# Performance work log

Measured on AMD Instinct MI355X. Metric: run time of the kernel, lower is better.

The kernel has to match this reference:

```python
import jax, jax.numpy as jnp
import numpy as np

N = 100000      # nodes
E = 1600000     # edges (avg degree 16)
IN = 64         # in_feats
OUT = 64        # out_feats per head
H = 4           # heads
SLOPE = 0.2     # leaky relu negative slope


def setup_inputs() -> dict:
    key = jax.random.key(0)
    ks = jax.random.split(key, 6)
    feat = jax.random.normal(ks[0], (N, IN), dtype=jnp.float32)
    # xavier-ish scale for weights
    W_weight = jax.random.normal(ks[1], (OUT * H, IN), dtype=jnp.float32) * (2.0 / (IN + OUT * H)) ** 0.5
    W_bias = jnp.zeros((OUT * H,), dtype=jnp.float32)
    a_l = jax.random.normal(ks[2], (1, OUT, H), dtype=jnp.float32) * 0.1
    a_r = jax.random.normal(ks[3], (1, OUT, H), dtype=jnp.float32) * 0.1
    row = jax.random.randint(ks[4], (E,), 0, N, dtype=jnp.int32)
    col = jax.random.randint(ks[5], (E,), 0, N, dtype=jnp.int32)
    return {"feat": feat, "W_weight": W_weight, "W_bias": W_bias,
            "a_l": a_l, "a_r": a_r, "row": row, "col": col}


def reference(feat, W_weight, W_bias, a_l, a_r, row, col):
    n = feat.shape[0]
    # linear projection -> [N, OUT, H]
    Z = (feat @ W_weight.T + W_bias).reshape(n, OUT, H)
    # per-node attention logits [N, H]
    e_l = (Z * a_l).sum(axis=1)
    e_r = (Z * a_r).sum(axis=1)
    # edge scores + leaky relu [E, H]
    e = e_l[row] + e_r[col]
    a = jnp.where(e > 0, e, SLOPE * e)
    # segment softmax over incoming edges of each destination row
    m = jax.ops.segment_max(a, row, num_segments=n)          # [N, H]
    ex = jnp.exp(a - m[row])                                  # [E, H]
    s = jax.ops.segment_sum(ex, row, num_segments=n)          # [N, H]
    alpha = ex / s[row]                                       # [E, H]
    # weighted aggregation: out[i,:,h] = sum_{e: row[e]=i} alpha[e,h] * Z[col[e],:,h]
    msg = alpha[:, None, :] * Z[col]                          # [E, OUT, H]
    out = jax.ops.segment_sum(msg, row, num_segments=n)       # [N, OUT, H]
    return out.reshape(n, -1)
```

## Files before the change

### kernel.cpp

```cpp
#include <hip/hip_runtime.h>
#include <stdint.h>

#define SLOPE  0.2f
#define PN     64
#define CAP    48
#define SCAP   16
#define SBMAX  512
#define ESMAX  3200
#define BINS   1600

typedef float    f32x4 __attribute__((ext_vector_type(4)));
typedef _Float16 h16x2 __attribute__((ext_vector_type(2)));

union FU { float f; unsigned int u; };
union HU { unsigned int u; h16x2 h; };
__device__ __forceinline__ float ubits(unsigned int u) { FU c; c.u = u; return c.f; }

__global__ __launch_bounds__(256) void front_kernel(
    const int* __restrict__ row, const int* __restrict__ col,
    int* __restrict__ cnt_sub,
    unsigned int* __restrict__ subreg,
    const float4* __restrict__ feat4, const float* __restrict__ W,
    const float* __restrict__ bias, const float* __restrict__ a_l,
    const float* __restrict__ a_r,
    uint2* __restrict__ featb2, float* __restrict__ el, float* __restrict__ er,
    unsigned int* __restrict__ WtHu, float* __restrict__ biasP,
    int E, int ES, int NBK, int N, int SC, int PJ)
{
    __shared__ char smemRaw[33024];

    int b = blockIdx.x;
    int t = threadIdx.x;

    if (b < SC) {
        unsigned int* stage = (unsigned int*)smemRaw;
        int* hist = (int*)(smemRaw + 12800);
        int* ofs  = (int*)(smemRaw + 19200);
        int* cur  = (int*)(smemRaw + 25600);
        int* part = (int*)(smemRaw + 32000);

        int blk = b;
        int e0 = blk * ES;
        int e1 = min(e0 + ES, E);
        int tot = e1 - e0;

        for (int p = t; p < BINS; p += 256) hist[p] = 0;
        __syncthreads();

        for (int e = e0 + t; e < e1; e += 256) {
            int r = __builtin_nontemporal_load(&row[e]);
            atomicAdd(&hist[r >> 6], 1);
        }
        __syncthreads();

        int lc[7]; int loc = 0;
        #pragma unroll
        for (int q = 0; q < 7; q++) {
            int bb = t * 7 + q;
            int v = (bb < BINS) ? hist[bb] : 0;
            lc[q] = loc; loc += v;
        }
        part[t] = loc;
        __syncthreads();
        for (int off = 1; off < 256; off <<= 1) {
            int v = (t >= off) ? part[t - off] : 0;
            __syncthreads();
            part[t] += v;
            __syncthreads();
        }
        int pbase = (t > 0) ? part[t - 1] : 0;
        #pragma unroll
        for (int q = 0; q < 7; q++) {
            int bb = t * 7 + q;
            if (bb < BINS) { ofs[bb] = pbase + lc[q]; cur[bb] = pbase + lc[q]; }
        }
        __syncthreads();

        for (int e = e0 + t; e < e1; e += 256) {
            int r = __builtin_nontemporal_load(&row[e]);
            int c = __builtin_nontemporal_load(&col[e]);
            int pos = atomicAdd(&cur[r >> 6], 1);
            stage[pos] = (unsigned)c | ((unsigned)(r & 63) << 20);
        }
        __syncthreads();

        unsigned int* dst = subreg + (size_t)blk * NBK * SCAP;
        int mx = max(tot - 1, 0);
        for (int p = t; p < NBK * SCAP; p += 256) {
            int bk = p >> 4, j = p & 15;
            int idx = ofs[bk] + j;
            dst[p] = stage[min(idx, mx)];
        }
        for (int p = t; p < NBK; p += 256)
            cnt_sub[(size_t)blk * NBK + p] = min(hist[p], SCAP);
        return;
    }
    if (b < SC + PJ) {
        float (*fT)[68]  = (float(*)[68])smemRaw;
        float (*WlS)[68] = (float(*)[68])(smemRaw + 17408);
        float* blS       = (float*)(smemRaw + 17408 + 2176);

        int nodeBase = (b - SC) * PN;

        for (int p = t; p < PN * 16; p += 256) {
            int n = p >> 4, kq = p & 15;
            int gn = nodeBase + n;
            float4 v = make_float4(0.f, 0.f, 0.f, 0.f);
            if (gn < N) v = feat4[(size_t)gn * 16 + kq];
            fT[kq * 4 + 0][n] = v.x; fT[kq * 4 + 1][n] = v.y;
            fT[kq * 4 + 2][n] = v.z; fT[kq * 4 + 3][n] = v.w;
            if (gn < N) {
                HU u0, u1;
                u0.h = (h16x2){ (_Float16)v.x, (_Float16)v.y };
                u1.h = (h16x2){ (_Float16)v.z, (_Float16)v.w };
                featb2[(size_t)gn * 16 + kq] = make_uint2(u0.u, u1.u);
            }
        }
        for (int r = 0; r < 2; r++) {
            int id = t + 256 * r;
            int x = id >> 6, k = id & 63, h = x & 3;
            const float* v = (x < 4) ? a_l : a_r;
            float s = 0.f;
            for (int d = 0; d < 64; d++) {
                int o = d * 4 + h;
                s += v[o] * W[o * 64 + k];
            }
            WlS[x][k] = s;
        }
        if (t < 8) {
            int h = t & 3;
            const float* v = (t < 4) ? a_l : a_r;
            float s = 0.f;
            for (int d = 0; d < 64; d++) { int o = d * 4 + h; s += v[o] * bias[o]; }
            blS[t] = s;
        }
        __syncthreads();

        for (int r = 0; r < 2; r++) {
            int id = t + 256 * r;
            int n = id >> 3, x = id & 7;
            int gn = nodeBase + n;
            if (gn < N) {
                float e = blS[x];
                #pragma unroll 8
                for (int k = 0; k < 64; k++) e += fT[k][n] * WlS[x][k];
                if (x < 4) el[(size_t)gn * 4 + x] = e;
                else       er[(size_t)gn * 4 + (x - 4)] = e;
            }
        }
        return;
    }
    if (b < SC + PJ + 32) {
        int g = (b - SC - PJ) * 256 + t;
        int kk = g >> 8, cp = g & 255;
        int o = (cp & 63) * 4 + (cp >> 6);
        HU u;
        u.h = (h16x2){ (_Float16)W[o * 64 + 2 * kk], (_Float16)W[o * 64 + 2 * kk + 1] };
        WtHu[kk * 256 + cp] = u.u;
        return;
    }
    {
        int cp = t;
        int o = (cp & 63) * 4 + (cp >> 6);
        biasP[cp] = bias[o];
    }
}

__global__ __launch_bounds__(1024) void gat_aggregate(
    const uint2* __restrict__ featb2,
    const float* __restrict__ el, const float* __restrict__ er,
    const int* __restrict__ cnt_sub, const unsigned int* __restrict__ subreg,
    uint2* __restrict__ agg, int* __restrict__ deg,
    int N, int NBK, int SB)
{
    __shared__ int      cntL[64];
    __shared__ unsigned listL[64 * CAP];
    __shared__ float    aL[16][64];
    __shared__ int      segC[SBMAX];

    int t = threadIdx.x, lane = t & 63, w = t >> 6;
    int bk = blockIdx.x;
    int nodeBase = bk << 6;

    for (int p = t; p < 64 * CAP / 4; p += 1024)
        *(uint4*)&listL[p * 4] = make_uint4(0u, 0u, 0u, 0u);
    if (t < 64) cntL[t] = 0;
    for (int p = t; p < SB; p += 1024) segC[p] = cnt_sub[(size_t)p * NBK + bk];
    __syncthreads();

    for (int p = t; p < SB * SCAP; p += 1024) {
        int blk = p >> 4, j = p & 15;
        if (j < segC[blk]) {
            unsigned wd = subreg[((size_t)blk * NBK + bk) * SCAP + j];
            int nl = wd >> 20;
            int pos = atomicAdd(&cntL[nl], 1);
            if (pos < CAP) listL[nl * CAP + pos] = wd & 0xFFFFFu;
        }
    }
    __syncthreads();

    int eL = lane >> 2, hh = lane & 3;
    int hsel = lane >> 4, kq = lane & 15;

    for (int u = 0; u < 4; u++) {
        int nl = w * 4 + u;
        int i = nodeBase + nl;
        if (i >= N) break;
        int dg = min(cntL[nl], CAP);
        const unsigned* lst = &listL[nl * CAP];
        float elh = el[i * 4 + hh];

        float m = -3.0e38f, m_h = -3.0e38f, l = 0.f;
        float a0 = 0.f, a1 = 0.f, a2 = 0.f, a3 = 0.f;

        for (int base = 0; base < dg; base += 16) {
            int cnt2 = min(16, dg - base);
            bool full = (cnt2 > 8);

            int c = (eL < cnt2) ? (int)lst[base + eL] : 0;
            float ev = er[c * 4 + hh];

            uint2 fq[16];
            #pragma unroll
            for (int jj = 0; jj < 2; jj++) {
                uint4 c4 = *(const uint4*)&lst[base + 4 * jj];
                fq[4 * jj + 0] = featb2[c4.x * 16 + kq];
                fq[4 * jj + 1] = featb2[c4.y * 16 + kq];
                fq[4 * jj + 2] = featb2[c4.z * 16 + kq];
                fq[4 * jj + 3] = featb2[c4.w * 16 + kq];
            }
            if (full) {
                #pragma unroll
                for (int jj = 2; jj < 4; jj++) {
                    uint4 c4 = *(const uint4*)&lst[base + 4 * jj];
                    fq[4 * jj + 0] = featb2[c4.x * 16 + kq];
                    fq[4 * jj + 1] = featb2[c4.y * 16 + kq];
                    fq[4 * jj + 2] = featb2[c4.z * 16 + kq];
                    fq[4 * jj + 3] = featb2[c4.w * 16 + kq];
                }
            }

            float e  = elh + ev;
            float sc = (eL < cnt2) ? (e > 0.f ? e : SLOPE * e) : -3.0e38f;
            float v = sc;
            v = fmaxf(v, __shfl_xor(v, 4));
            v = fmaxf(v, __shfl_xor(v, 8));
            v = fmaxf(v, __shfl_xor(v, 16));
            v = fmaxf(v, __shfl_xor(v, 32));
            float mnew = fmaxf(m, v);
            float a = __expf(sc - mnew);
            float sv = a;
            sv += __shfl_xor(sv, 4);
            sv += __shfl_xor(sv, 8);
            sv += __shfl_xor(sv, 16);
            sv += __shfl_xor(sv, 32);
            l = l * __expf(m - mnew) + sv;
            m = mnew;

            aL[w][hh * 16 + eL] = a;

            float mn_h = __shfl(mnew, hsel);
            float r = __expf(m_h - mn_h);
            a0 *= r; a1 *= r; a2 *= r; a3 *= r;
            m_h = mn_h;

            #pragma unroll
            for (int jj = 0; jj < 2; jj++) {
                f32x4 al4 = *(const f32x4*)&aL[w][hsel * 16 + 4 * jj];
                #pragma unroll
                for (int q = 0; q < 4; q++) {
                    float al = al4[q];
                    HU hx, hy; hx.u = fq[4 * jj + q].x; hy.u = fq[4 * jj + q].y;
                    a0 += al * (float)hx.h[0];
                    a1 += al * (float)hx.h[1];
                    a2 += al * (float)hy.h[0];
                    a3 += al * (float)hy.h[1];
                }
            }
            if (full) {
                #pragma unroll
                for (int jj = 2; jj < 4; jj++) {
                    f32x4 al4 = *(const f32x4*)&aL[w][hsel * 16 + 4 * jj];
                    #pragma unroll
                    for (int q = 0; q < 4; q++) {
                        float al = al4[q];
                        HU hx, hy; hx.u = fq[4 * jj + q].x; hy.u = fq[4 * jj + q].y;
                        a0 += al * (float)hx.h[0];
                        a1 += al * (float)hx.h[1];
                        a2 += al * (float)hy.h[0];
                        a3 += al * (float)hy.h[1];
                    }
                }
            }
        }

        float lh  = __shfl(l, hsel);
        float inv = (lh > 0.f) ? 1.0f / lh : 0.f;
        HU p0, p1;
        p0.h = (h16x2){ (_Float16)(a0 * inv), (_Float16)(a1 * inv) };
        p1.h = (h16x2){ (_Float16)(a2 * inv), (_Float16)(a3 * inv) };
        agg[(unsigned)(i * 64 + lane)] = make_uint2(p0.u, p1.u);
    }

    __syncthreads();
    if (t < 64) {
        int i = nodeBase + t;
        if (i < N) deg[i] = min(cntL[t], CAP);
    }
}

__global__ __launch_bounds__(256) void gemm_kernel(
    const uint4* __restrict__ agg4,
    const uint4* __restrict__ WtH4,
    const float* __restrict__ biasP,
    const int* __restrict__ deg,
    float* __restrict__ out, int N)
{
    __shared__ char smem[32768 + 17408 + 128];
    unsigned int* WtS   = (unsigned int*)smem;
    unsigned int* aggSu = (unsigned int*)(smem + 32768);
    int*          degS  = (int*)(smem + 32768 + 17408);
    float*        obS   = (float*)smem;

    int t = threadIdx.x;
    int nodeBase = blockIdx.x * 32;

    #pragma unroll
    for (int p = 0; p < 8; p++)
        *(uint4*)&WtS[(p * 256 + t) * 4] = WtH4[p * 256 + t];
    for (int p = t; p < 1024; p += 256) {
        int n = p >> 5, q = p & 31;
        int gn = nodeBase + n;
        uint4 v = make_uint4(0u, 0u, 0u, 0u);
        if (gn < N) v = agg4[(size_t)gn * 32 + q];
        *(uint4*)&aggSu[n * 132 + q * 4] = v;
    }
    if (t < 32) { int gn = nodeBase + t; degS[t] = (gn < N) ? deg[gn] : 0; }
    __syncthreads();

    int cg = t & 31, ng = t >> 5;
    int h = cg >> 3;
    float acc[4][8];
    #pragma unroll
    for (int u = 0; u < 4; u++)
        #pragma unroll
        for (int j = 0; j < 8; j++) acc[u][j] = 0.f;

    for (int kk = 0; kk < 32; kk++) {
        uint4 wv0 = *(const uint4*)&WtS[kk * 256 + cg * 8];
        uint4 wv1 = *(const uint4*)&WtS[kk * 256 + cg * 8 + 4];
        unsigned int au[4];
        #pragma unroll
        for (int u = 0; u < 4; u++)
            au[u] = aggSu[(ng * 4 + u) * 132 + h * 32 + kk];
        HU wp[8];
        wp[0].u = wv0.x; wp[1].u = wv0.y; wp[2].u = wv0.z; wp[3].u = wv0.w;
        wp[4].u = wv1.x; wp[5].u = wv1.y; wp[6].u = wv1.z; wp[7].u = wv1.w;
        #pragma unroll
        for (int u = 0; u < 4; u++) {
            HU av; av.u = au[u];
            #pragma unroll
            for (int j = 0; j < 8; j++)
                acc[u][j] = __builtin_amdgcn_fdot2(av.h, wp[j].h, acc[u][j], false);
        }
    }

    float4 b0 = *(const float4*)&biasP[cg * 8];
    float4 b1 = *(const float4*)&biasP[cg * 8 + 4];
    float bj[8] = { b0.x, b0.y, b0.z, b0.w, b1.x, b1.y, b1.z, b1.w };
    int bq[4];
    #pragma unroll
    for (int u = 0; u < 4; u++) bq[u] = degS[ng * 4 + u];
    __syncthreads();

    #pragma unroll
    for (int u = 0; u < 4; u++) {
        int n = ng * 4 + u;
        float bsc = (bq[u] > 0) ? 1.f : 0.f;
        f32x4 x0 = { acc[u][0] + bsc * bj[0], acc[u][1] + bsc * bj[1],
                     acc[u][2] + bsc * bj[2], acc[u][3] + bsc * bj[3] };
        f32x4 x1 = { acc[u][4] + bsc * bj[4], acc[u][5] + bsc * bj[5],
                     acc[u][6] + bsc * bj[6], acc[u][7] + bsc * bj[7] };
        *(f32x4*)&obS[n * 264 + cg * 8]     = x0;
        *(f32x4*)&obS[n * 264 + cg * 8 + 4] = x1;
    }
    __syncthreads();

    int ln = t >> 3, part = t & 7;
    int gn = nodeBase + ln;
    if (gn < N) {
        #pragma unroll
        for (int k = 0; k < 8; k++) {
            int d = k * 8 + part;
            f32x4 o4 = { obS[ln * 264 +   0 + d], obS[ln * 264 +  64 + d],
                         obS[ln * 264 + 128 + d], obS[ln * 264 + 192 + d] };
            __builtin_nontemporal_store(o4, (f32x4*)(out + (size_t)gn * 256) + d);
        }
    }
}

extern "C" void kernel_launch(void* const* d_in, const int* in_sizes, int n_in,
                              void* d_out, int out_size, void* d_ws, size_t ws_size,
                              hipStream_t stream)
{
    const float* feat  = (const float*)d_in[0];
    const float* W     = (const float*)d_in[1];
    const float* bias  = (const float*)d_in[2];
    const float* a_l   = (const float*)d_in[3];
    const float* a_r   = (const float*)d_in[4];
    const int*   row   = (const int*)d_in[5];
    const int*   col   = (const int*)d_in[6];
    float* out = (float*)d_out;

    int N = in_sizes[0] / 64;
    int E = in_sizes[5];

    char* ws = (char*)d_ws;
    size_t off = 0;
    auto alloc = [&](size_t bytes) -> void* {
        void* p = (void*)(ws + off);
        off += (bytes + 255) & ~(size_t)255;
        return p;
    };
    int NBK = (N + 63) >> 6;
    int SB  = (E + 3124) / 3125;
    if (SB > SBMAX) SB = SBMAX;
    int ES  = (E + SB - 1) / SB;

    unsigned short* featb = (unsigned short*)alloc((size_t)N * 64 * sizeof(unsigned short));
    unsigned int*   WtHu  = (unsigned int*)alloc(8192 * sizeof(unsigned int));
    float*          biasP = (float*)alloc(256 * sizeof(float));
    float* el      = (float*)alloc((size_t)N * 4 * sizeof(float));
    float* er      = (float*)alloc((size_t)N * 4 * sizeof(float));
    int*   cnt_sub = (int*)alloc((size_t)SB * NBK * sizeof(int));
    unsigned int* subreg = (unsigned int*)alloc((size_t)SB * NBK * SCAP * sizeof(unsigned int));
    uint2* agg     = (uint2*)alloc((size_t)N * 64 * sizeof(uint2));
    int*   deg     = (int*)alloc((size_t)N * sizeof(int));
    (void)ws_size; (void)n_in; (void)out_size;

    int PJ = (N + PN - 1) / PN;
    int SC = SB;

    front_kernel<<<SC + PJ + 33, 256, 0, stream>>>(
        row, col, cnt_sub, subreg, (const float4*)feat, W, bias, a_l, a_r,
        (uint2*)featb, el, er, WtHu, biasP, E, ES, NBK, N, SC, PJ);
    gat_aggregate<<<NBK, 1024, 0, stream>>>(
        (const uint2*)featb, el, er, cnt_sub, subreg, agg, deg, N, NBK, SB);
    gemm_kernel<<<(N + 31) / 32, 256, 0, stream>>>(
        (const uint4*)agg, (const uint4*)WtHu, biasP, deg, out, N);
}
```

Baseline: 320.1 us.

## Split bucket compaction into separate kernel and aggregate one node per wave

Moves the per-block gathering of edge sub-buckets into a new compact_kernel that writes a padded per-node neighbor list (CAP slots) and degrees to global memory. The aggregation kernel then runs one wavefront per node in small 256-thread blocks. It stages neighbor indices through a tiny shared buffer and prefetches the next chunk's indices. The aim is better occupancy and load balance than the 1024-thread blocks that carried large shared lists. The cost is an extra kernel launch and a global round trip of the padded CSR array.

```diff
diff --git a/kernel.cpp b/kernel.cpp
--- a/kernel.cpp
+++ b/kernel.cpp
@@ -166,29 +166,24 @@
     }
 }
 
-__global__ __launch_bounds__(1024) void gat_aggregate(
-    const uint2* __restrict__ featb2,
-    const float* __restrict__ el, const float* __restrict__ er,
+__global__ __launch_bounds__(256) void compact_kernel(
     const int* __restrict__ cnt_sub, const unsigned int* __restrict__ subreg,
-    uint2* __restrict__ agg, int* __restrict__ deg,
-    int N, int NBK, int SB)
+    int* __restrict__ csr, int* __restrict__ deg, int N, int NBK, int SB)
 {
     __shared__ int      cntL[64];
     __shared__ unsigned listL[64 * CAP];
-    __shared__ float    aL[16][64];
     __shared__ int      segC[SBMAX];
 
-    int t = threadIdx.x, lane = t & 63, w = t >> 6;
-    int bk = blockIdx.x;
+    int t = threadIdx.x, bk = blockIdx.x;
     int nodeBase = bk << 6;
 
-    for (int p = t; p < 64 * CAP / 4; p += 1024)
+    for (int p = t; p < 64 * CAP / 4; p += 256)
         *(uint4*)&listL[p * 4] = make_uint4(0u, 0u, 0u, 0u);
     if (t < 64) cntL[t] = 0;
-    for (int p = t; p < SB; p += 1024) segC[p] = cnt_sub[(size_t)p * NBK + bk];
+    for (int p = t; p < SB; p += 256) segC[p] = cnt_sub[(size_t)p * NBK + bk];
     __syncthreads();
 
-    for (int p = t; p < SB * SCAP; p += 1024) {
+    for (int p = t; p < SB * SCAP; p += 256) {
         int blk = p >> 4, j = p & 15;
         if (j < segC[blk]) {
             unsigned wd = subreg[((size_t)blk * NBK + bk) * SCAP + j];
@@ -199,73 +194,114 @@
     }
     __syncthreads();
 
+    int4* dst = (int4*)(csr + (size_t)nodeBase * CAP);
+    for (int p = t; p < 64 * CAP / 4; p += 256)
+        dst[p] = *(int4*)&listL[p * 4];
+    if (t < 64) {
+        int i = nodeBase + t;
+        if (i < N) deg[i] = min(cntL[t], CAP);
+    }
+}
+
+__global__ __launch_bounds__(256) void gat_aggregate(
+    const uint2* __restrict__ featb2,
+    const float* __restrict__ el, const float* __restrict__ er,
+    const int* __restrict__ deg, const int* __restrict__ csr,
+    uint2* __restrict__ agg, int N)
+{
+    __shared__ float aL[4][64];
+    __shared__ int   cL[4][16];
+
+    int t = threadIdx.x, lane = t & 63, w = t >> 6;
+    int i = blockIdx.x * 4 + w;
+    if (i >= N) return;
+
+    int start = i * CAP;
+    int dg = deg[i];
     int eL = lane >> 2, hh = lane & 3;
     int hsel = lane >> 4, kq = lane & 15;
-
-    for (int u = 0; u < 4; u++) {
-        int nl = w * 4 + u;
-        int i = nodeBase + nl;
-        if (i >= N) break;
-        int dg = min(cntL[nl], CAP);
-        const unsigned* lst = &listL[nl * CAP];
-        float elh = el[i * 4 + hh];
-
-        float m = -3.0e38f, m_h = -3.0e38f, l = 0.f;
-        float a0 = 0.f, a1 = 0.f, a2 = 0.f, a3 = 0.f;
-
-        for (int base = 0; base < dg; base += 16) {
-            int cnt2 = min(16, dg - base);
-            bool full = (cnt2 > 8);
-
-            int c = (eL < cnt2) ? (int)lst[base + eL] : 0;
-            float ev = er[c * 4 + hh];
-
-            uint2 fq[16];
+    float elh = el[i * 4 + hh];
+
+    float m = -3.0e38f;
+    float m_h = -3.0e38f;
+    float l = 0.f;
+    float a0 = 0.f, a1 = 0.f, a2 = 0.f, a3 = 0.f;
+
+    int c = 0;
+    if (eL < dg) c = csr[start + eL];
+
+    for (int base = 0; base < dg; base += 16) {
+        int cnt2 = min(16, dg - base);
+        bool full = (cnt2 > 8);
+
+        if (hh == 0) cL[w][eL] = c;
+
+        float ev = er[c * 4 + hh];
+
+        uint2 fq[16];
+        #pragma unroll
+        for (int jj = 0; jj < 2; jj++) {
+            int4 c4 = *(const int4*)&cL[w][4 * jj];
+            fq[4 * jj + 0] = featb2[(unsigned)(c4.x * 16 + kq)];
+            fq[4 * jj + 1] = featb2[(unsigned)(c4.y * 16 + kq)];
+            fq[4 * jj + 2] = featb2[(unsigned)(c4.z * 16 + kq)];
+            fq[4 * jj + 3] = featb2[(unsigned)(c4.w * 16 + kq)];
+        }
+        if (full) {
             #pragma unroll
-            for (int jj = 0; jj < 2; jj++) {
-                uint4 c4 = *(const uint4*)&lst[base + 4 * jj];
-                fq[4 * jj + 0] = featb2[c4.x * 16 + kq];
-                fq[4 * jj + 1] = featb2[c4.y * 16 + kq];
-                fq[4 * jj + 2] = featb2[c4.z * 16 + kq];
-                fq[4 * jj + 3] = featb2[c4.w * 16 + kq];
-            }
-            if (full) {
-                #pragma unroll
-                for (int jj = 2; jj < 4; jj++) {
-                    uint4 c4 = *(const uint4*)&lst[base + 4 * jj];
-                    fq[4 * jj + 0] = featb2[c4.x * 16 + kq];
-                    fq[4 * jj + 1] = featb2[c4.y * 16 + kq];
-                    fq[4 * jj + 2] = featb2[c4.z * 16 + kq];
-                    fq[4 * jj + 3] = featb2[c4.w * 16 + kq];
-                }
-            }
-
-            float e  = elh + ev;
-            float sc = (eL < cnt2) ? (e > 0.f ? e : SLOPE * e) : -3.0e38f;
-            float v = sc;
-            v = fmaxf(v, __shfl_xor(v, 4));
-            v = fmaxf(v, __shfl_xor(v, 8));
-            v = fmaxf(v, __shfl_xor(v, 16));
-            v = fmaxf(v, __shfl_xor(v, 32));
-            float mnew = fmaxf(m, v);
-            float a = __expf(sc - mnew);
-            float sv = a;
-            sv += __shfl_xor(sv, 4);
-            sv += __shfl_xor(sv, 8);
-            sv += __shfl_xor(sv, 16);
-            sv += __shfl_xor(sv, 32);
-            l = l * __expf(m - mnew) + sv;
-            m = mnew;
-
-            aL[w][hh * 16 + eL] = a;
-
-            float mn_h = __shfl(mnew, hsel);
-            float r = __expf(m_h - mn_h);
-            a0 *= r; a1 *= r; a2 *= r; a3 *= r;
-            m_h = mn_h;
-
+            for (int jj = 2; jj < 4; jj++) {
+                int4 c4 = *(const int4*)&cL[w][4 * jj];
+                fq[4 * jj + 0] = featb2[(unsigned)(c4.x * 16 + kq)];
+                fq[4 * jj + 1] = featb2[(unsigned)(c4.y * 16 + kq)];
+                fq[4 * jj + 2] = featb2[(unsigned)(c4.z * 16 + kq)];
+                fq[4 * jj + 3] = featb2[(unsigned)(c4.w * 16 + kq)];
+            }
+        }
+
+        int rem = dg - base - 16;
+        int cn = 0;
+        if (rem > 0 && eL < rem) cn = csr[start + base + 16 + eL];
+
+        float e  = elh + ev;
+        float sc = (eL < cnt2) ? (e > 0.f ? e : SLOPE * e) : -3.0e38f;
+        float v = sc;
+        v = fmaxf(v, __shfl_xor(v, 4));
+        v = fmaxf(v, __shfl_xor(v, 8));
+        v = fmaxf(v, __shfl_xor(v, 16));
+        v = fmaxf(v, __shfl_xor(v, 32));
+        float mnew = fmaxf(m, v);
+        float a = __expf(sc - mnew);
+        float sv = a;
+        sv += __shfl_xor(sv, 4);
+        sv += __shfl_xor(sv, 8);
+        sv += __shfl_xor(sv, 16);
+        sv += __shfl_xor(sv, 32);
+        l = l * __expf(m - mnew) + sv;
+        m = mnew;
+
+        aL[w][hh * 16 + eL] = a;
+
+        float mn_h = __shfl(mnew, hsel);
+        float r = __expf(m_h - mn_h);
+        a0 *= r; a1 *= r; a2 *= r; a3 *= r;
+        m_h = mn_h;
+
+        #pragma unroll
+        for (int jj = 0; jj < 2; jj++) {
+            f32x4 al4 = *(const f32x4*)&aL[w][hsel * 16 + 4 * jj];
             #pragma unroll
-            for (int jj = 0; jj < 2; jj++) {
+            for (int q = 0; q < 4; q++) {
+                float al = al4[q];
+                HU hx, hy; hx.u = fq[4 * jj + q].x; hy.u = fq[4 * jj + q].y;
+                a0 += al * (float)hx.h[0];
+                a1 += al * (float)hx.h[1];
+                a2 += al * (float)hy.h[0];
+                a3 += al * (float)hy.h[1];
+            }
+        }
+        if (full) {
+            #pragma unroll
+            for (int jj = 2; jj < 4; jj++) {
                 f32x4 al4 = *(const f32x4*)&aL[w][hsel * 16 + 4 * jj];
                 #pragma unroll
                 for (int q = 0; q < 4; q++) {
@@ -277,36 +313,16 @@
                     a3 += al * (float)hy.h[1];
                 }
             }
-            if (full) {
-                #pragma unroll
-                for (int jj = 2; jj < 4; jj++) {
-                    f32x4 al4 = *(const f32x4*)&aL[w][hsel * 16 + 4 * jj];
-                    #pragma unroll
-                    for (int q = 0; q < 4; q++) {
-                        float al = al4[q];
-                        HU hx, hy; hx.u = fq[4 * jj + q].x; hy.u = fq[4 * jj + q].y;
-                        a0 += al * (float)hx.h[0];
-                        a1 += al * (float)hx.h[1];
-                        a2 += al * (float)hy.h[0];
-                        a3 += al * (float)hy.h[1];
-                    }
-                }
-            }
-        }
-
-        float lh  = __shfl(l, hsel);
-        float inv = (lh > 0.f) ? 1.0f / lh : 0.f;
-        HU p0, p1;
-        p0.h = (h16x2){ (_Float16)(a0 * inv), (_Float16)(a1 * inv) };
-        p1.h = (h16x2){ (_Float16)(a2 * inv), (_Float16)(a3 * inv) };
-        agg[(unsigned)(i * 64 + lane)] = make_uint2(p0.u, p1.u);
-    }
-
-    __syncthreads();
-    if (t < 64) {
-        int i = nodeBase + t;
-        if (i < N) deg[i] = min(cntL[t], CAP);
-    }
+        }
+        c = cn;
+    }
+
+    float lh  = __shfl(l, hsel);
+    float inv = (lh > 0.f) ? 1.0f / lh : 0.f;
+    HU p0, p1;
+    p0.h = (h16x2){ (_Float16)(a0 * inv), (_Float16)(a1 * inv) };
+    p1.h = (h16x2){ (_Float16)(a2 * inv), (_Float16)(a3 * inv) };
+    agg[(unsigned)(i * 64 + lane)] = make_uint2(p0.u, p1.u);
 }
 
 __global__ __launch_bounds__(256) void gemm_kernel(
@@ -434,8 +450,9 @@
     float* er      = (float*)alloc((size_t)N * 4 * sizeof(float));
     int*   cnt_sub = (int*)alloc((size_t)SB * NBK * sizeof(int));
     unsigned int* subreg = (unsigned int*)alloc((size_t)SB * NBK * SCAP * sizeof(unsigned int));
+    int*   csr     = (int*)alloc((size_t)NBK * 64 * CAP * sizeof(int));
+    int*   deg     = (int*)alloc((size_t)N * sizeof(int));
     uint2* agg     = (uint2*)alloc((size_t)N * 64 * sizeof(uint2));
-    int*   deg     = (int*)alloc((size_t)N * sizeof(int));
     (void)ws_size; (void)n_in; (void)out_size;
 
     int PJ = (N + PN - 1) / PN;
@@ -444,8 +461,9 @@
     front_kernel<<<SC + PJ + 33, 256, 0, stream>>>(
         row, col, cnt_sub, subreg, (const float4*)feat, W, bias, a_l, a_r,
         (uint2*)featb, el, er, WtHu, biasP, E, ES, NBK, N, SC, PJ);
-    gat_aggregate<<<NBK, 1024, 0, stream>>>(
-        (const uint2*)featb, el, er, cnt_sub, subreg, agg, deg, N, NBK, SB);
+    compact_kernel<<<NBK, 256, 0, stream>>>(cnt_sub, subreg, csr, deg, N, NBK, SB);
+    gat_aggregate<<<(N + 3) / 4, 256, 0, stream>>>(
+        (const uint2*)featb, el, er, deg, csr, agg, N);
     gemm_kernel<<<(N + 31) / 32, 256, 0, stream>>>(
         (const uint4*)agg, (const uint4*)WtHu, biasP, deg, out, N);
 }
```

New measurement: 290.7 us. 1.1x faster.
